# Optimization experiments

Hardware: AMD Instinct MI355X
Metric: run time of the kernel (lower is better)

The kernel has to match this reference:

```python
import jax, jax.numpy as jnp
import numpy as np

N, T, E, D, U = 32, 2048, 512, 1024, 256


def setup_inputs() -> dict:
    key = jax.random.key(0)
    ks = jax.random.split(key, 6)
    queries = jax.random.normal(ks[0], (N, 1, D), dtype=jnp.float32)
    prev = jax.random.uniform(ks[1], (N, T), dtype=jnp.float32)
    prev = prev / jnp.sum(prev, axis=1, keepdims=True)  # distribution-like initial alignment
    memory = jax.random.normal(ks[2], (N, T, E), dtype=jnp.float32)
    W_q = jax.random.normal(ks[3], (D, U), dtype=jnp.float32) * (1.0 / np.sqrt(D))
    W_k = jax.random.normal(ks[4], (E, U), dtype=jnp.float32) * (1.0 / np.sqrt(E))
    v = jax.random.uniform(ks[5], (U,), dtype=jnp.float32)
    return {"queries": queries, "previous_alignments": prev, "memory": memory,
            "W_q": W_q, "W_k": W_k, "v": v}


def safe_cumprod_exclusive(x):
    # exclusive cumprod via log-space cumsum, clamped like the torch original
    logsum = jnp.cumsum(jnp.log(jnp.clip(x, 1e-20, 1.0)), axis=1)  # [N,T]
    excl = jnp.concatenate([jnp.zeros_like(logsum[:, :1]), logsum], axis=1)[:, :-1]
    return jnp.exp(excl)


def reference(queries, previous_alignments, memory, W_q, W_k, v):
    # Bahdanau additive score (normalize=False path)
    proj_key = jnp.einsum('bte,eu->btu', memory, W_k)          # set_memory
    proj_q = jnp.einsum('bqd,du->bqu', queries, W_q)           # [N,1,U]
    weights = jnp.einsum('btu,u->bt', jnp.tanh(proj_q + proj_key), v)  # [N,T]
    p_choose = jax.nn.sigmoid(weights)
    # monotonic attention recursion in cumsum/cumprod form
    cumprod_1mp = safe_cumprod_exclusive(1.0 - p_choose)
    alignments = p_choose * cumprod_1mp * jnp.cumsum(
        previous_alignments / jnp.clip(cumprod_1mp, 1e-10, 1.0), axis=1)
    contexts = jnp.einsum('bt,bte->be', alignments, memory)    # bmm + squeeze
    return (contexts, alignments)
```

## Files before the change

kernel.cpp:

```cpp
#include <hip/hip_runtime.h>
#include <math.h>

#define N_ 32
#define T_ 2048
#define E_ 512
#define D_ 1024
#define U_ 256

typedef __attribute__((ext_vector_type(8))) short bf16x8;
typedef __attribute__((ext_vector_type(16))) float f32x16;

__device__ __forceinline__ short f2bf_rne(float x) {
  unsigned int u = __float_as_uint(x);
  unsigned int r = u + 0x7FFFu + ((u >> 16) & 1u);
  return (short)(r >> 16);
}
__device__ __forceinline__ short f2bf_trunc(float x) {
  return (short)(__float_as_uint(x) >> 16);
}
__device__ __forceinline__ float bf2f(short h) {
  return __uint_as_float(((unsigned int)(unsigned short)h) << 16);
}
__device__ __forceinline__ float fast_tanh(float x) {
  float t = exp2f(x * 2.8853900817779268f);
  return 1.0f - 2.0f * __builtin_amdgcn_rcpf(t + 1.0f);
}
__device__ __forceinline__ float fast_sigmoid(float w) {
  return __builtin_amdgcn_rcpf(1.0f + exp2f(-1.4426950408889634f * w));
}

__global__ __launch_bounds__(256) void prep_kernel(
    const float* __restrict__ Wk, const float* __restrict__ queries,
    const float* __restrict__ Wq, bf16x8* __restrict__ whiP,
    bf16x8* __restrict__ wloP, float* __restrict__ pq_part) {
  const int wg = blockIdx.x, tid = threadIdx.x;
  if (wg < 64) {
    const int fid = wg * 256 + tid;
    const int lane = fid & 63;
    const int ub = (fid >> 6) & 7;
    const int kc = (fid >> 9) & 3;
    const int c = fid >> 11;
    const int u = ub * 32 + (lane & 31);
    const int e0 = c * 64 + kc * 16 + (lane >> 5) * 8;
    bf16x8 H, L;
#pragma unroll
    for (int j = 0; j < 8; ++j) {
      float x = Wk[(size_t)(e0 + j) * U_ + u];
      short h = f2bf_trunc(x);
      H[j] = h;
      L[j] = f2bf_rne(x - bf2f(h));
    }
    whiP[fid] = H;
    wloP[fid] = L;
  } else {
    const int ch = (wg - 64) & 3;
    const int bb = (wg - 64) >> 2;
    const int d0 = ch * 256;
    const float* q = queries + bb * D_ + d0;
    const float* wq = Wq + (size_t)d0 * U_ + tid;
    float acc = 0.f;
#pragma unroll 8
    for (int d = 0; d < 256; ++d)
      acc = fmaf(q[d], wq[(size_t)d * U_], acc);
    pq_part[(bb * 4 + ch) * U_ + tid] = acc;
  }
}

__global__ __launch_bounds__(256, 2) void score_kernel(
    const float* __restrict__ memory, const bf16x8* __restrict__ whiP,
    const bf16x8* __restrict__ wloP, const float* __restrict__ pq_part,
    const float* __restrict__ v, float* __restrict__ p_choose) {
  __shared__ short sAhi[128 * 64];
  __shared__ short sAlo[128 * 64];
  __shared__ float smem_w[4][128];

  const int b = blockIdx.y;
  const int t0 = blockIdx.x * 128;
  const int tid = threadIdx.x;
  const int lane = tid & 63;
  const int ty = tid >> 6;
  const int l31 = lane & 31;
  const int half = lane >> 5;

  f32x16 acc[4][2];
#pragma unroll
  for (int mt = 0; mt < 4; ++mt)
#pragma unroll
    for (int nt = 0; nt < 2; ++nt)
#pragma unroll
      for (int r = 0; r < 16; ++r) acc[mt][nt][r] = 0.f;

  const int sr = tid >> 1;
  const int cs = (tid & 1) * 32;
  const float* srow = memory + ((size_t)(b * T_ + t0 + sr)) * E_ + cs;

  for (int it = 0; it < 8; ++it) {
    float4 xr[8];
    const float* src = srow + it * 64;
#pragma unroll
    for (int j = 0; j < 8; ++j) xr[j] = *(const float4*)(src + j * 4);
    __syncthreads();
    {
      char* bhp = (char*)sAhi + sr * 128;
      char* blp = (char*)sAlo + sr * 128;
#pragma unroll
      for (int j = 0; j < 4; ++j) {
        float xs[8] = {xr[2 * j].x, xr[2 * j].y, xr[2 * j].z, xr[2 * j].w,
                       xr[2 * j + 1].x, xr[2 * j + 1].y, xr[2 * j + 1].z, xr[2 * j + 1].w};
        bf16x8 H, L;
#pragma unroll
        for (int i = 0; i < 8; ++i) {
          short h = f2bf_trunc(xs[i]);
          H[i] = h;
          L[i] = f2bf_rne(xs[i] - bf2f(h));
        }
        const int slot = (((tid & 1) * 4 + j) ^ (sr & 7)) * 16;
        *(bf16x8*)(bhp + slot) = H;
        *(bf16x8*)(blp + slot) = L;
      }
    }
    __syncthreads();

#pragma unroll
    for (int kc = 0; kc < 4; ++kc) {
      bf16x8 bh[2], bl[2];
#pragma unroll
      for (int nt = 0; nt < 2; ++nt) {
        const int fidx = ((it * 4 + kc) * 8 + (ty * 2 + nt)) * 64 + lane;
        bh[nt] = whiP[fidx];
        bl[nt] = wloP[fidx];
      }
      bf16x8 ah[4], al[4];
#pragma unroll
      for (int mt = 0; mt < 4; ++mt) {
        const int m = mt * 32 + l31;
        const int off = m * 128 + (((kc * 2 + half) ^ (m & 7)) * 16);
        ah[mt] = *(const bf16x8*)((const char*)sAhi + off);
        al[mt] = *(const bf16x8*)((const char*)sAlo + off);
      }
#pragma unroll
      for (int mt = 0; mt < 4; ++mt)
#pragma unroll
        for (int nt = 0; nt < 2; ++nt) {
          acc[mt][nt] = __builtin_amdgcn_mfma_f32_32x32x16_bf16(ah[mt], bh[nt], acc[mt][nt], 0, 0, 0);
          acc[mt][nt] = __builtin_amdgcn_mfma_f32_32x32x16_bf16(ah[mt], bl[nt], acc[mt][nt], 0, 0, 0);
          acc[mt][nt] = __builtin_amdgcn_mfma_f32_32x32x16_bf16(al[mt], bh[nt], acc[mt][nt], 0, 0, 0);
        }
    }
  }

  const int u0 = ty * 64 + l31;
  const int u1 = u0 + 32;
  float pq0 = 0.f, pq1 = 0.f;
#pragma unroll
  for (int c = 0; c < 4; ++c) {
    pq0 += pq_part[(b * 4 + c) * U_ + u0];
    pq1 += pq_part[(b * 4 + c) * U_ + u1];
  }
  const float v0 = v[u0], v1 = v[u1];
#pragma unroll
  for (int mt = 0; mt < 4; ++mt)
#pragma unroll
    for (int r = 0; r < 16; ++r) {
      float s = fast_tanh(acc[mt][0][r] + pq0) * v0 + fast_tanh(acc[mt][1][r] + pq1) * v1;
#pragma unroll
      for (int off = 1; off < 32; off <<= 1) s += __shfl_xor(s, off, 64);
      if (l31 == 0) {
        const int row = mt * 32 + (r & 3) + 8 * (r >> 2) + 4 * half;
        smem_w[ty][row] = s;
      }
    }
  __syncthreads();
  if (tid < 128) {
    const float w = smem_w[0][tid] + smem_w[1][tid] + smem_w[2][tid] + smem_w[3][tid];
    p_choose[b * T_ + t0 + tid] = fast_sigmoid(w);
  }
}

__device__ __forceinline__ float block_incl_scan(float val, float* sbuf, int tid) {
  float x = val;
  sbuf[tid] = x;
  __syncthreads();
#pragma unroll
  for (int off = 1; off < 256; off <<= 1) {
    float t = (tid >= off) ? sbuf[tid - off] : 0.f;
    __syncthreads();
    x += t;
    sbuf[tid] = x;
    __syncthreads();
  }
  return x;
}

__global__ __launch_bounds__(256) void scan_kernel(
    const float* __restrict__ p_choose, const float* __restrict__ prev,
    float* __restrict__ align_out, float* __restrict__ ctx_out) {
  __shared__ float sbuf[256];
  const int b = blockIdx.x, tid = threadIdx.x;
  ctx_out[b * E_ + tid] = 0.f;
  ctx_out[b * E_ + 256 + tid] = 0.f;
  const int base = b * T_ + tid * 8;
  float4 p0 = *(const float4*)(p_choose + base);
  float4 p1 = *(const float4*)(p_choose + base + 4);
  float p[8] = {p0.x, p0.y, p0.z, p0.w, p1.x, p1.y, p1.z, p1.w};
  float s[8];
  float run = 0.f;
#pragma unroll
  for (int k = 0; k < 8; ++k) {
    float x = 1.0f - p[k];
    x = fminf(fmaxf(x, 1e-20f), 1.0f);
    run += logf(x);
    s[k] = run;
  }
  float incl = block_incl_scan(run, sbuf, tid);
  float excl = incl - run;
  float cp[8];
#pragma unroll
  for (int k = 0; k < 8; ++k)
    cp[k] = expf(excl + (k ? s[k - 1] : 0.f));
  float4 r0 = *(const float4*)(prev + base);
  float4 r1 = *(const float4*)(prev + base + 4);
  float pr[8] = {r0.x, r0.y, r0.z, r0.w, r1.x, r1.y, r1.z, r1.w};
  float s2[8];
  float run2 = 0.f;
#pragma unroll
  for (int k = 0; k < 8; ++k) {
    float d = fminf(fmaxf(cp[k], 1e-10f), 1.0f);
    run2 += pr[k] / d;
    s2[k] = run2;
  }
  float incl2 = block_incl_scan(run2, sbuf, tid);
  float excl2 = incl2 - run2;
#pragma unroll
  for (int k = 0; k < 8; ++k)
    p[k] = p[k] * cp[k] * (excl2 + s2[k]);
  *(float4*)(align_out + base) = make_float4(p[0], p[1], p[2], p[3]);
  *(float4*)(align_out + base + 4) = make_float4(p[4], p[5], p[6], p[7]);
}

__global__ __launch_bounds__(256) void ctx_kernel(
    const float* __restrict__ memory, const float* __restrict__ align,
    float* __restrict__ ctx_out) {
  const int wg = blockIdx.x, tid = threadIdx.x;
  const int b = wg >> 4;
  const int t0 = (wg & 15) * 128 + (tid >> 7) * 64;
  const int col = (tid & 127) * 4;
  const float* mrow = memory + ((size_t)(b * T_ + t0)) * E_ + col;
  const float* arow = align + b * T_ + t0;
  float4 a = make_float4(0.f, 0.f, 0.f, 0.f);
  for (int t = 0; t < 64; t += 4) {
    float4 m0 = *(const float4*)(mrow + (size_t)(t + 0) * E_);
    float4 m1 = *(const float4*)(mrow + (size_t)(t + 1) * E_);
    float4 m2 = *(const float4*)(mrow + (size_t)(t + 2) * E_);
    float4 m3 = *(const float4*)(mrow + (size_t)(t + 3) * E_);
    float a0 = arow[t], a1 = arow[t + 1], a2 = arow[t + 2], a3 = arow[t + 3];
    a.x = fmaf(a0, m0.x, a.x); a.y = fmaf(a0, m0.y, a.y);
    a.z = fmaf(a0, m0.z, a.z); a.w = fmaf(a0, m0.w, a.w);
    a.x = fmaf(a1, m1.x, a.x); a.y = fmaf(a1, m1.y, a.y);
    a.z = fmaf(a1, m1.z, a.z); a.w = fmaf(a1, m1.w, a.w);
    a.x = fmaf(a2, m2.x, a.x); a.y = fmaf(a2, m2.y, a.y);
    a.z = fmaf(a2, m2.z, a.z); a.w = fmaf(a2, m2.w, a.w);
    a.x = fmaf(a3, m3.x, a.x); a.y = fmaf(a3, m3.y, a.y);
    a.z = fmaf(a3, m3.z, a.z); a.w = fmaf(a3, m3.w, a.w);
  }
  float* dst = ctx_out + b * E_ + col;
  atomicAdd(dst + 0, a.x);
  atomicAdd(dst + 1, a.y);
  atomicAdd(dst + 2, a.z);
  atomicAdd(dst + 3, a.w);
}

extern "C" void kernel_launch(void* const* d_in, const int* in_sizes, int n_in,
                              void* d_out, int out_size, void* d_ws, size_t ws_size,
                              hipStream_t stream) {
  (void)in_sizes; (void)n_in; (void)out_size; (void)ws_size;
  const float* queries = (const float*)d_in[0];
  const float* prev    = (const float*)d_in[1];
  const float* memory  = (const float*)d_in[2];
  const float* Wq      = (const float*)d_in[3];
  const float* Wk      = (const float*)d_in[4];
  const float* v       = (const float*)d_in[5];

  float* out = (float*)d_out;
  float* ctx_out = out;
  float* align_out = out + N_ * E_;

  float* ws = (float*)d_ws;
  bf16x8* whiP    = (bf16x8*)ws;
  bf16x8* wloP    = (bf16x8*)(ws + 65536);
  float* p_choose = ws + 131072;
  float* pq_part  = ws + 196608;

  prep_kernel<<<dim3(64 + 128), 256, 0, stream>>>(Wk, queries, Wq, whiP, wloP, pq_part);
  score_kernel<<<dim3(T_ / 128, N_), 256, 0, stream>>>(memory, whiP, wloP, pq_part, v, p_choose);
  scan_kernel<<<dim3(N_), 256, 0, stream>>>(p_choose, prev, align_out, ctx_out);
  ctx_kernel<<<dim3(512), 256, 0, stream>>>(memory, align_out, ctx_out);
}
```

Measured before the change: 278.3 us.

## Load memory fragments directly into MFMA registers, dropping LDS staging

The score kernel no longer stages the fp32 memory tile through shared memory as split bf16 hi/lo halves. Each wave now reads its A fragments straight from global memory in the MFMA operand layout and converts them in registers. This removes the LDS writes, LDS reads and both barriers per K-chunk. In exchange, each of the four waves in the block loads and converts the same 128xE tile itself, giving four times the global/L2 traffic and the conversion work. It also uses more strided 32-byte accesses per lane.

Result: slower. 316.1 us (+13.6%).

```diff
diff --git a/kernel.cpp b/kernel.cpp
--- a/kernel.cpp
+++ b/kernel.cpp
@@ -70,8 +70,6 @@
     const float* __restrict__ memory, const bf16x8* __restrict__ whiP,
     const bf16x8* __restrict__ wloP, const float* __restrict__ pq_part,
     const float* __restrict__ v, float* __restrict__ p_choose) {
-  __shared__ short sAhi[128 * 64];
-  __shared__ short sAlo[128 * 64];
   __shared__ float smem_w[4][128];
 
   const int b = blockIdx.y;
@@ -90,63 +88,45 @@
 #pragma unroll
       for (int r = 0; r < 16; ++r) acc[mt][nt][r] = 0.f;
 
-  const int sr = tid >> 1;
-  const int cs = (tid & 1) * 32;
-  const float* srow = memory + ((size_t)(b * T_ + t0 + sr)) * E_ + cs;
-
-  for (int it = 0; it < 8; ++it) {
-    float4 xr[8];
-    const float* src = srow + it * 64;
-#pragma unroll
-    for (int j = 0; j < 8; ++j) xr[j] = *(const float4*)(src + j * 4);
-    __syncthreads();
-    {
-      char* bhp = (char*)sAhi + sr * 128;
-      char* blp = (char*)sAlo + sr * 128;
-#pragma unroll
-      for (int j = 0; j < 4; ++j) {
-        float xs[8] = {xr[2 * j].x, xr[2 * j].y, xr[2 * j].z, xr[2 * j].w,
-                       xr[2 * j + 1].x, xr[2 * j + 1].y, xr[2 * j + 1].z, xr[2 * j + 1].w};
-        bf16x8 H, L;
-#pragma unroll
-        for (int i = 0; i < 8; ++i) {
-          short h = f2bf_trunc(xs[i]);
-          H[i] = h;
-          L[i] = f2bf_rne(xs[i] - bf2f(h));
-        }
-        const int slot = (((tid & 1) * 4 + j) ^ (sr & 7)) * 16;
-        *(bf16x8*)(bhp + slot) = H;
-        *(bf16x8*)(blp + slot) = L;
+  const float* aptr = memory + ((size_t)(b * T_ + t0 + l31)) * E_ + half * 8;
+  const bf16x8* bhp = whiP + (size_t)(ty * 2) * 64 + lane;
+  const bf16x8* blp = wloP + (size_t)(ty * 2) * 64 + lane;
+
+#pragma unroll 2
+  for (int step = 0; step < 32; ++step) {
+    float4 a0[4], a1[4];
+#pragma unroll
+    for (int mt = 0; mt < 4; ++mt) {
+      const float* p = aptr + (size_t)mt * (32 * E_) + step * 16;
+      a0[mt] = *(const float4*)(p);
+      a1[mt] = *(const float4*)(p + 4);
+    }
+    bf16x8 bh[2], bl[2];
+#pragma unroll
+    for (int nt = 0; nt < 2; ++nt) {
+      bh[nt] = bhp[(size_t)(step * 8 + nt) * 64];
+      bl[nt] = blp[(size_t)(step * 8 + nt) * 64];
+    }
+    bf16x8 ah[4], al[4];
+#pragma unroll
+    for (int mt = 0; mt < 4; ++mt) {
+      float xs[8] = {a0[mt].x, a0[mt].y, a0[mt].z, a0[mt].w,
+                     a1[mt].x, a1[mt].y, a1[mt].z, a1[mt].w};
+#pragma unroll
+      for (int i = 0; i < 8; ++i) {
+        short h = f2bf_trunc(xs[i]);
+        ah[mt][i] = h;
+        al[mt][i] = f2bf_rne(xs[i] - bf2f(h));
       }
     }
-    __syncthreads();
-
-#pragma unroll
-    for (int kc = 0; kc < 4; ++kc) {
-      bf16x8 bh[2], bl[2];
+#pragma unroll
+    for (int mt = 0; mt < 4; ++mt)
 #pragma unroll
       for (int nt = 0; nt < 2; ++nt) {
-        const int fidx = ((it * 4 + kc) * 8 + (ty * 2 + nt)) * 64 + lane;
-        bh[nt] = whiP[fidx];
-        bl[nt] = wloP[fidx];
+        acc[mt][nt] = __builtin_amdgcn_mfma_f32_32x32x16_bf16(ah[mt], bh[nt], acc[mt][nt], 0, 0, 0);
+        acc[mt][nt] = __builtin_amdgcn_mfma_f32_32x32x16_bf16(ah[mt], bl[nt], acc[mt][nt], 0, 0, 0);
+        acc[mt][nt] = __builtin_amdgcn_mfma_f32_32x32x16_bf16(al[mt], bh[nt], acc[mt][nt], 0, 0, 0);
       }
-      bf16x8 ah[4], al[4];
-#pragma unroll
-      for (int mt = 0; mt < 4; ++mt) {
-        const int m = mt * 32 + l31;
-        const int off = m * 128 + (((kc * 2 + half) ^ (m & 7)) * 16);
-        ah[mt] = *(const bf16x8*)((const char*)sAhi + off);
-        al[mt] = *(const bf16x8*)((const char*)sAlo + off);
-      }
-#pragma unroll
-      for (int mt = 0; mt < 4; ++mt)
-#pragma unroll
-        for (int nt = 0; nt < 2; ++nt) {
-          acc[mt][nt] = __builtin_amdgcn_mfma_f32_32x32x16_bf16(ah[mt], bh[nt], acc[mt][nt], 0, 0, 0);
-          acc[mt][nt] = __builtin_amdgcn_mfma_f32_32x32x16_bf16(ah[mt], bl[nt], acc[mt][nt], 0, 0, 0);
-          acc[mt][nt] = __builtin_amdgcn_mfma_f32_32x32x16_bf16(al[mt], bh[nt], acc[mt][nt], 0, 0, 0);
-        }
-    }
   }
 
   const int u0 = ty * 64 + l31;
```

## Double-buffer score kernel LDS staging with prefetch of next memory chunk

Applied to the files above, without the earlier changes.

The score GEMM staging changes from 8 iterations of 64-wide K chunks with two barriers each to 16 iterations of 32-wide chunks in a double-buffered LDS array holding hi and lo halves together. The next chunk's global loads are issued before the MFMAs on the current buffer, and the bf16 split and store go into the other buffer afterwards. This leaves one barrier per iteration and lets global load latency overlap compute. In exchange there are twice as many iterations, fewer bytes in flight per thread, and the total LDS footprint stays the same.

Result: faster. 268.8 us (-3.4%).

```diff
diff --git a/kernel.cpp b/kernel.cpp
--- a/kernel.cpp
+++ b/kernel.cpp
@@ -70,8 +70,7 @@
     const float* __restrict__ memory, const bf16x8* __restrict__ whiP,
     const bf16x8* __restrict__ wloP, const float* __restrict__ pq_part,
     const float* __restrict__ v, float* __restrict__ p_choose) {
-  __shared__ short sAhi[128 * 64];
-  __shared__ short sAlo[128 * 64];
+  __shared__ short sA[2][128 * 64];
   __shared__ float smem_w[4][128];
 
   const int b = blockIdx.y;
@@ -91,52 +90,65 @@
       for (int r = 0; r < 16; ++r) acc[mt][nt][r] = 0.f;
 
   const int sr = tid >> 1;
-  const int cs = (tid & 1) * 32;
+  const int cs = (tid & 1) * 16;
+  const int s0 = cs >> 3;
+  const int sw = sr & 7;
   const float* srow = memory + ((size_t)(b * T_ + t0 + sr)) * E_ + cs;
-
-  for (int it = 0; it < 8; ++it) {
-    float4 xr[8];
-    const float* src = srow + it * 64;
-#pragma unroll
-    for (int j = 0; j < 8; ++j) xr[j] = *(const float4*)(src + j * 4);
-    __syncthreads();
-    {
-      char* bhp = (char*)sAhi + sr * 128;
-      char* blp = (char*)sAlo + sr * 128;
-#pragma unroll
-      for (int j = 0; j < 4; ++j) {
-        float xs[8] = {xr[2 * j].x, xr[2 * j].y, xr[2 * j].z, xr[2 * j].w,
-                       xr[2 * j + 1].x, xr[2 * j + 1].y, xr[2 * j + 1].z, xr[2 * j + 1].w};
-        bf16x8 H, L;
-#pragma unroll
-        for (int i = 0; i < 8; ++i) {
-          short h = f2bf_trunc(xs[i]);
-          H[i] = h;
-          L[i] = f2bf_rne(xs[i] - bf2f(h));
-        }
-        const int slot = (((tid & 1) * 4 + j) ^ (sr & 7)) * 16;
-        *(bf16x8*)(bhp + slot) = H;
-        *(bf16x8*)(blp + slot) = L;
-      }
-    }
-    __syncthreads();
-
-#pragma unroll
-    for (int kc = 0; kc < 4; ++kc) {
+  char* const bp0 = (char*)&sA[0][0] + sr * 128;
+  char* const bp1 = (char*)&sA[1][0] + sr * 128;
+
+  float4 xr[4];
+#pragma unroll
+  for (int j = 0; j < 4; ++j) xr[j] = *(const float4*)(srow + j * 4);
+
+  auto do_stage = [&](char* bp) {
+    float xs[16] = {xr[0].x, xr[0].y, xr[0].z, xr[0].w,
+                    xr[1].x, xr[1].y, xr[1].z, xr[1].w,
+                    xr[2].x, xr[2].y, xr[2].z, xr[2].w,
+                    xr[3].x, xr[3].y, xr[3].z, xr[3].w};
+    bf16x8 H0, H1, L0, L1;
+#pragma unroll
+    for (int i = 0; i < 8; ++i) {
+      short h0 = f2bf_trunc(xs[i]);
+      H0[i] = h0;
+      L0[i] = f2bf_rne(xs[i] - bf2f(h0));
+      short h1 = f2bf_trunc(xs[8 + i]);
+      H1[i] = h1;
+      L1[i] = f2bf_rne(xs[8 + i] - bf2f(h1));
+    }
+    *(bf16x8*)(bp + (((s0 + 0) ^ sw) * 16)) = H0;
+    *(bf16x8*)(bp + (((s0 + 1) ^ sw) * 16)) = H1;
+    *(bf16x8*)(bp + (((s0 + 4) ^ sw) * 16)) = L0;
+    *(bf16x8*)(bp + (((s0 + 5) ^ sw) * 16)) = L1;
+  };
+
+  do_stage(bp0);
+  __syncthreads();
+
+  int cur = 0;
+  for (int it = 0; it < 16; ++it) {
+    if (it < 15) {
+      const float* src = srow + (it + 1) * 32;
+#pragma unroll
+      for (int j = 0; j < 4; ++j) xr[j] = *(const float4*)(src + j * 4);
+    }
+    const char* base = (const char*)&sA[cur][0];
+#pragma unroll
+    for (int kc = 0; kc < 2; ++kc) {
       bf16x8 bh[2], bl[2];
 #pragma unroll
       for (int nt = 0; nt < 2; ++nt) {
-        const int fidx = ((it * 4 + kc) * 8 + (ty * 2 + nt)) * 64 + lane;
+        const int fidx = ((it * 2 + kc) * 8 + (ty * 2 + nt)) * 64 + lane;
         bh[nt] = whiP[fidx];
         bl[nt] = wloP[fidx];
       }
+      const int sl = kc * 2 + half;
       bf16x8 ah[4], al[4];
 #pragma unroll
       for (int mt = 0; mt < 4; ++mt) {
         const int m = mt * 32 + l31;
-        const int off = m * 128 + (((kc * 2 + half) ^ (m & 7)) * 16);
-        ah[mt] = *(const bf16x8*)((const char*)sAhi + off);
-        al[mt] = *(const bf16x8*)((const char*)sAlo + off);
+        ah[mt] = *(const bf16x8*)(base + (size_t)m * 128 + ((sl ^ (m & 7)) * 16));
+        al[mt] = *(const bf16x8*)(base + (size_t)m * 128 + (((sl + 4) ^ (m & 7)) * 16));
       }
 #pragma unroll
       for (int mt = 0; mt < 4; ++mt)
@@ -147,6 +159,9 @@
           acc[mt][nt] = __builtin_amdgcn_mfma_f32_32x32x16_bf16(al[mt], bh[nt], acc[mt][nt], 0, 0, 0);
         }
     }
+    if (it < 15) do_stage(cur ? bp0 : bp1);
+    __syncthreads();
+    cur ^= 1;
   }
 
   const int u0 = ty * 64 + l31;
```
